# Kernel tuning notes

Measured on AMD Instinct MI355X. Metric: run time of the kernel, lower is better.

## Reference

```python
import jax, jax.numpy as jnp
import numpy as np

NUM_AGENTS = 16


def setup_inputs() -> dict:
    key = jax.random.key(0)
    ks = jax.random.split(key, 9)
    B, N, C = 64, 1024, 512
    w_scale = 1.0 / np.sqrt(C)  # keep pre-softmax logits in a sane range
    return {
        "x": jax.random.normal(ks[0], (B, N, C), dtype=jnp.float32),
        "Wq": jax.random.normal(ks[1], (C, C), dtype=jnp.float32) * w_scale,
        "bq": jax.random.normal(ks[2], (C,), dtype=jnp.float32) * 0.02,
        "Wk": jax.random.normal(ks[3], (C, C), dtype=jnp.float32) * w_scale,
        "bk": jax.random.normal(ks[4], (C,), dtype=jnp.float32) * 0.02,
        "Wv": jax.random.normal(ks[5], (C, C), dtype=jnp.float32) * w_scale,
        "bv": jax.random.normal(ks[6], (C,), dtype=jnp.float32) * 0.02,
        "Wo": jax.random.normal(ks[7], (C, C), dtype=jnp.float32) * w_scale,
        "bo": jax.random.normal(ks[8], (C,), dtype=jnp.float32) * 0.02,
    }


def reference(x, Wq, bq, Wk, bk, Wv, bv, Wo, bo):
    B, N, C = x.shape
    M = NUM_AGENTS
    scale = C ** (-0.5)
    # torch nn.Linear: y = x @ W.T + b
    Q = jnp.einsum('bnc,dc->bnd', x, Wq) + bq  # [B,N,C]
    K = jnp.einsum('bnc,dc->bnd', x, Wk) + bk
    V = jnp.einsum('bnc,dc->bnd', x, Wv) + bv
    # adaptive_avg_pool1d over token dim; N % M == 0 -> mean over groups of N//M
    A = Q.reshape(B, M, N // M, C).mean(axis=2)  # [B,M,C]
    # stage 1: softmax(Q A^T)
    agent_tokens = jax.nn.softmax(jnp.einsum('bnc,bmc->bnm', Q, A) * scale, axis=-1)  # [B,N,M]
    # stage 2: softmax(A K^T) V
    agent_features = jax.nn.softmax(jnp.einsum('bmc,bnc->bmn', A, K) * scale, axis=-1)  # [B,M,N]
    agent_features = jnp.einsum('bmn,bnc->bmc', agent_features, V)  # [B,M,C]
    # combine
    agent_attn = jnp.einsum('bnm,bmc->bnc', agent_tokens, agent_features)  # [B,N,C]
    return jnp.einsum('bnc,dc->bnd', agent_attn, Wo) + bo
```

## Files before the change

### kernel.cpp

```cpp
#include <hip/hip_runtime.h>

#define BB 64
#define NN 1024
#define CC 512
#define MM 16
#define SCALE 0.04419417382415922f

__device__ __forceinline__ float dot4(float4 a, float4 b) {
  return a.x*b.x + a.y*b.y + a.z*b.z + a.w*b.w;
}

__global__ void k_pool2(const float* __restrict__ x, float* __restrict__ P) {
  __shared__ float4 tmp[128];
  int blk = blockIdx.x;
  int t = threadIdx.x;
  int c4 = t & 127, h = t >> 7;
  const float4* base = (const float4*)(x + (size_t)blk * 64 * CC);
  float4 a = {0.f,0.f,0.f,0.f};
  #pragma unroll 8
  for (int i = 0; i < 32; ++i) {
    float4 v = base[(size_t)(h*32 + i)*128 + c4];
    a.x += v.x; a.y += v.y; a.z += v.z; a.w += v.w;
  }
  if (h == 1) tmp[c4] = a;
  __syncthreads();
  if (h == 0) {
    float4 o = tmp[c4];
    const float inv = 1.0f/64.0f;
    float4 r = {(a.x+o.x)*inv, (a.y+o.y)*inv, (a.z+o.z)*inv, (a.w+o.w)*inv};
    ((float4*)P)[(size_t)blk*128 + c4] = r;
  }
}

__global__ void k_gemm_nt(const float* __restrict__ In, const float* __restrict__ W,
                          const float* __restrict__ bias, float* __restrict__ Out) {
  int t = threadIdx.x;
  int tx = t & 15, ty = t >> 4;
  int r0 = blockIdx.y*32 + ty*2;
  int d0 = blockIdx.x*32 + tx*2;
  const float4* In4 = (const float4*)In;
  const float4* W4  = (const float4*)W;
  float acc00=0.f, acc01=0.f, acc10=0.f, acc11=0.f;
  for (int c4 = 0; c4 < 128; ++c4) {
    float4 a0 = In4[(size_t)r0*128 + c4];
    float4 a1 = In4[(size_t)(r0+1)*128 + c4];
    float4 w0 = W4[(size_t)d0*128 + c4];
    float4 w1 = W4[(size_t)(d0+1)*128 + c4];
    acc00 += dot4(a0,w0); acc01 += dot4(a0,w1);
    acc10 += dot4(a1,w0); acc11 += dot4(a1,w1);
  }
  float b0 = bias[d0], b1 = bias[d0+1];
  float2 o0 = {acc00+b0, acc01+b1};
  float2 o1 = {acc10+b0, acc11+b1};
  *(float2*)(Out + (size_t)r0*CC + d0) = o0;
  *(float2*)(Out + (size_t)(r0+1)*CC + d0) = o1;
}

__global__ void k_abqk(const float* __restrict__ A, const float* __restrict__ bq,
                       const float* __restrict__ bk, float* __restrict__ abq,
                       float* __restrict__ abk) {
  int bm = blockIdx.x, t = threadIdx.x;
  float sq = 0.f, sk = 0.f;
  for (int d = t; d < CC; d += 64) {
    float a = A[(size_t)bm*CC + d];
    sq += a*bq[d]; sk += a*bk[d];
  }
  #pragma unroll
  for (int off = 32; off >= 1; off >>= 1) {
    sq += __shfl_xor(sq, off);
    sk += __shfl_xor(sk, off);
  }
  if (t == 0) { abq[bm] = sq; abk[bm] = sk; }
}

__global__ void k_gemm_nn2(const float* __restrict__ A, const float* __restrict__ Wq,
                           const float* __restrict__ Wk, float* __restrict__ Aq,
                           float* __restrict__ Ak) {
  int t = threadIdx.x;
  int tx = t & 15, ty = t >> 4;
  int r0 = blockIdx.y*32 + ty*2;
  int c0 = blockIdx.x*32 + tx*2;
  float q00=0.f,q01=0.f,q10=0.f,q11=0.f;
  float k00=0.f,k01=0.f,k10=0.f,k11=0.f;
  #pragma unroll 4
  for (int d = 0; d < CC; ++d) {
    float a0 = A[(size_t)r0*CC + d];
    float a1 = A[(size_t)(r0+1)*CC + d];
    float2 wq = *(const float2*)(Wq + (size_t)d*CC + c0);
    float2 wk = *(const float2*)(Wk + (size_t)d*CC + c0);
    q00 += a0*wq.x; q01 += a0*wq.y; q10 += a1*wq.x; q11 += a1*wq.y;
    k00 += a0*wk.x; k01 += a0*wk.y; k10 += a1*wk.x; k11 += a1*wk.y;
  }
  float2 v;
  v.x=q00; v.y=q01; *(float2*)(Aq + (size_t)r0*CC + c0) = v;
  v.x=q10; v.y=q11; *(float2*)(Aq + (size_t)(r0+1)*CC + c0) = v;
  v.x=k00; v.y=k01; *(float2*)(Ak + (size_t)r0*CC + c0) = v;
  v.x=k10; v.y=k11; *(float2*)(Ak + (size_t)(r0+1)*CC + c0) = v;
}

__global__ __launch_bounds__(128) void k_logits3(
    const float* __restrict__ x, const float* __restrict__ Aq,
    const float* __restrict__ Ak, const float* __restrict__ abq,
    const float* __restrict__ abk, float* __restrict__ PT,
    float* __restrict__ E, float* __restrict__ dpart) {
  __shared__ float4 xs[128*17];
  __shared__ float ds[MM*132];
  __shared__ float ds2[MM*8];
  int b = blockIdx.y, t = threadIdx.x;
  int n0 = blockIdx.x*128;
  int n = n0 + t;
  const float4* Aq4 = (const float4*)(Aq + (size_t)b*MM*CC);
  const float4* Ak4 = (const float4*)(Ak + (size_t)b*MM*CC);
  const float4* xg  = (const float4*)(x + ((size_t)b*NN + n0)*CC);
  float aq[MM], ak[MM];
  #pragma unroll
  for (int m = 0; m < MM; ++m) { aq[m] = 0.f; ak[m] = 0.f; }
  for (int ch = 0; ch < 8; ++ch) {
    __syncthreads();
    #pragma unroll
    for (int j = 0; j < 16; ++j) {
      int i = j*128 + t;
      int row = i >> 4, col = i & 15;
      xs[row*17 + col] = xg[(size_t)row*128 + ch*16 + col];
    }
    __syncthreads();
    int cb = ch*16;
    #pragma unroll 4
    for (int c4 = 0; c4 < 16; ++c4) {
      float4 xv = xs[t*17 + c4];
      #pragma unroll
      for (int m = 0; m < MM; ++m) {
        aq[m] += dot4(xv, Aq4[m*128 + cb + c4]);
        ak[m] += dot4(xv, Ak4[m*128 + cb + c4]);
      }
    }
  }
  float mx = -1e30f;
  #pragma unroll
  for (int m = 0; m < MM; ++m) {
    aq[m] = SCALE*(aq[m] + abq[b*MM + m]);
    mx = fmaxf(mx, aq[m]);
  }
  float s = 0.f;
  #pragma unroll
  for (int m = 0; m < MM; ++m) { aq[m] = expf(aq[m]-mx); s += aq[m]; }
  float inv = 1.0f/s;
  float4* PT4 = (float4*)(PT + ((size_t)b*NN + n)*MM);
  #pragma unroll
  for (int j = 0; j < 4; ++j) {
    float4 v = {aq[j*4+0]*inv, aq[j*4+1]*inv, aq[j*4+2]*inv, aq[j*4+3]*inv};
    PT4[j] = v;
  }
  #pragma unroll
  for (int m = 0; m < MM; ++m) {
    float e = expf(SCALE*(ak[m] + abk[b*MM + m]));
    E[((size_t)b*MM + m)*NN + n] = e;
    ds[m*132 + t] = e;
  }
  __syncthreads();
  {
    int m2 = t >> 3, j2 = t & 7;
    float p = 0.f;
    #pragma unroll
    for (int i = 0; i < 16; ++i) p += ds[m2*132 + j2*16 + i];
    ds2[m2*8 + j2] = p;
  }
  __syncthreads();
  if (t < MM) {
    float d = 0.f;
    #pragma unroll
    for (int j = 0; j < 8; ++j) d += ds2[t*8 + j];
    dpart[((size_t)blockIdx.x*BB + b)*MM + t] = d;
  }
}

__global__ __launch_bounds__(256) void k_sacc3(const float* __restrict__ x,
                                               const float* __restrict__ E,
                                               float* __restrict__ Spart) {
  __shared__ float Es[MM*128];
  __shared__ float4 comb[MM*128];
  int ns = blockIdx.x, b = blockIdx.y, t = threadIdx.x;
  int col = t & 127, h = t >> 7;
  {
    const float4* E4 = (const float4*)E;
    float4* Es4 = (float4*)Es;
    #pragma unroll
    for (int k = 0; k < 2; ++k) {
      int i = k*256 + t;
      int m = i >> 5, j = i & 31;
      Es4[m*32 + j] = E4[((size_t)b*MM + m)*256 + ns*32 + j];
    }
  }
  __syncthreads();
  float4 acc[MM];
  #pragma unroll
  for (int m = 0; m < MM; ++m) acc[m] = make_float4(0.f,0.f,0.f,0.f);
  const float4* xb = (const float4*)(x + ((size_t)b*NN + ns*128 + h*64)*CC);
  for (int nl = 0; nl < 64; ++nl) {
    float4 xv = xb[(size_t)nl*128 + col];
    #pragma unroll
    for (int m = 0; m < MM; ++m) {
      float p = Es[m*128 + h*64 + nl];
      acc[m].x += p*xv.x; acc[m].y += p*xv.y; acc[m].z += p*xv.z; acc[m].w += p*xv.w;
    }
  }
  if (h == 1) {
    #pragma unroll
    for (int m = 0; m < MM; ++m) comb[m*128 + col] = acc[m];
  }
  __syncthreads();
  if (h == 0) {
    float4* Sp4 = (float4*)Spart;
    #pragma unroll
    for (int m = 0; m < MM; ++m) {
      float4 c = comb[m*128 + col];
      float4 r = {acc[m].x+c.x, acc[m].y+c.y, acc[m].z+c.z, acc[m].w+c.w};
      Sp4[(((size_t)ns*BB + b)*MM + m)*128 + col] = r;
    }
  }
}

__global__ void k_sreduce2(const float* __restrict__ Spart,
                           const float* __restrict__ dpart,
                           float* __restrict__ S) {
  int idx = blockIdx.x*256 + threadIdx.x;
  int row = idx >> 7;
  const float4* Sp4 = (const float4*)Spart;
  float4 a = {0.f,0.f,0.f,0.f};
  #pragma unroll
  for (int ns = 0; ns < 8; ++ns) {
    float4 v = Sp4[((size_t)ns*NN + row)*128 + (idx & 127)];
    a.x += v.x; a.y += v.y; a.z += v.z; a.w += v.w;
  }
  float d = 0.f;
  #pragma unroll
  for (int ns = 0; ns < 8; ++ns) d += dpart[(size_t)ns*NN + row];
  float inv = 1.0f/d;
  float4 r = {a.x*inv, a.y*inv, a.z*inv, a.w*inv};
  ((float4*)S)[idx] = r;
}

__global__ __launch_bounds__(128) void k_final3(const float* __restrict__ PT,
                                                const float* __restrict__ G,
                                                float* __restrict__ out) {
  int nc = blockIdx.x, b = blockIdx.y, t = threadIdx.x;
  float4 g[MM];
  const float4* G4 = (const float4*)(G + (size_t)b*MM*CC);
  #pragma unroll
  for (int m = 0; m < MM; ++m) g[m] = G4[m*128 + t];
  int n0 = nc*32;
  float4* out4 = (float4*)(out + ((size_t)b*NN + n0)*CC);
  const float* pt = PT + ((size_t)b*NN + n0)*MM;
  for (int i = 0; i < 32; ++i) {
    float4 o = {0.f,0.f,0.f,0.f};
    #pragma unroll
    for (int m = 0; m < MM; ++m) {
      float p = pt[i*MM + m];
      o.x += p*g[m].x; o.y += p*g[m].y; o.z += p*g[m].z; o.w += p*g[m].w;
    }
    out4[(size_t)i*128 + t] = o;
  }
}

extern "C" void kernel_launch(void* const* d_in, const int* in_sizes, int n_in,
                              void* d_out, int out_size, void* d_ws, size_t ws_size,
                              hipStream_t stream) {
  (void)in_sizes; (void)n_in; (void)out_size; (void)ws_size;
  const float* x  = (const float*)d_in[0];
  const float* Wq = (const float*)d_in[1];
  const float* bq = (const float*)d_in[2];
  const float* Wk = (const float*)d_in[3];
  const float* bk = (const float*)d_in[4];
  const float* Wv = (const float*)d_in[5];
  const float* bv = (const float*)d_in[6];
  const float* Wo = (const float*)d_in[7];
  const float* bo = (const float*)d_in[8];
  float* out = (float*)d_out;

  float* ws  = (float*)d_ws;
  float* P     = ws;
  float* A     = P  + 1024*512;
  float* Aq    = A  + 1024*512;
  float* Ak    = Aq + 1024*512;
  float* abq   = Ak + 1024*512;
  float* abk   = abq + 1024;
  float* PT    = abk + 1024;
  float* E     = PT + 1024*1024;
  float* dpart = E  + 1024*1024;
  float* S     = dpart + 8*1024;
  float* AF    = S  + 1024*512;
  float* G     = AF + 1024*512;
  float* Spart = G  + 1024*512;

  k_pool2<<<1024, 256, 0, stream>>>(x, P);
  k_gemm_nt<<<dim3(16,32), 256, 0, stream>>>(P, Wq, bq, A);
  k_abqk<<<1024, 64, 0, stream>>>(A, bq, bk, abq, abk);
  k_gemm_nn2<<<dim3(16,32), 256, 0, stream>>>(A, Wq, Wk, Aq, Ak);
  k_logits3<<<dim3(8,64), 128, 0, stream>>>(x, Aq, Ak, abq, abk, PT, E, dpart);
  k_sacc3<<<dim3(8,64), 256, 0, stream>>>(x, E, Spart);
  k_sreduce2<<<512, 256, 0, stream>>>(Spart, dpart, S);
  k_gemm_nt<<<dim3(16,32), 256, 0, stream>>>(S, Wv, bv, AF);
  k_gemm_nt<<<dim3(16,32), 256, 0, stream>>>(AF, Wo, bo, G);
  k_final3<<<dim3(32,64), 128, 0, stream>>>(PT, G, out);
}
```

Baseline: 760.5 us.

## Split logits over channel chunks, move softmax into sacc, retile small GEMMs

The logits kernel is split across four channel chunks (grid z) that write partial Q/K logits, which raises parallelism beyond 512 blocks. The softmax, exp and denominator work moves into the S-accumulation kernel, which sums the partials, so the E buffer round trip is gone. The small GEMMs are rewritten to stage input rows in shared memory with more blocks and coalesced weight reads. The final kernel uses smaller token chunks for more blocks. The cost is extra partial-logit traffic and redundant reloading of x per channel chunk.

Result: no change. 759.0 us (-0.2%).

```diff
diff --git a/kernel.cpp b/kernel.cpp
--- a/kernel.cpp
+++ b/kernel.cpp
@@ -8,6 +8,9 @@
 
 __device__ __forceinline__ float dot4(float4 a, float4 b) {
   return a.x*b.x + a.y*b.y + a.z*b.z + a.w*b.w;
+}
+__device__ __forceinline__ void fma4(float4& acc, float s, float4 v) {
+  acc.x += s*v.x; acc.y += s*v.y; acc.z += s*v.z; acc.w += s*v.w;
 }
 
 __global__ void k_pool2(const float* __restrict__ x, float* __restrict__ P) {
@@ -32,28 +35,35 @@
   }
 }
 
-__global__ void k_gemm_nt(const float* __restrict__ In, const float* __restrict__ W,
-                          const float* __restrict__ bias, float* __restrict__ Out) {
+__global__ __launch_bounds__(256) void k_gemm_nt3(const float* __restrict__ In,
+    const float* __restrict__ W, const float* __restrict__ bias,
+    float* __restrict__ Out) {
+  __shared__ float4 As[8*128];
   int t = threadIdx.x;
-  int tx = t & 15, ty = t >> 4;
-  int r0 = blockIdx.y*32 + ty*2;
-  int d0 = blockIdx.x*32 + tx*2;
+  int rblk = blockIdx.y, dblk = blockIdx.x;
   const float4* In4 = (const float4*)In;
-  const float4* W4  = (const float4*)W;
-  float acc00=0.f, acc01=0.f, acc10=0.f, acc11=0.f;
+  #pragma unroll
+  for (int k = 0; k < 4; ++k) {
+    int i = k*256 + t;
+    As[i] = In4[(size_t)(rblk*8 + (i>>7))*128 + (i&127)];
+  }
+  __syncthreads();
+  int d = dblk*64 + (t & 63);
+  int rr = t >> 6;
+  const float4* Wr = (const float4*)W + (size_t)d*128;
+  const float4* A0 = &As[(rr*2)*128];
+  const float4* A1 = &As[(rr*2+1)*128];
+  float acc0 = 0.f, acc1 = 0.f;
+  #pragma unroll 4
   for (int c4 = 0; c4 < 128; ++c4) {
-    float4 a0 = In4[(size_t)r0*128 + c4];
-    float4 a1 = In4[(size_t)(r0+1)*128 + c4];
-    float4 w0 = W4[(size_t)d0*128 + c4];
-    float4 w1 = W4[(size_t)(d0+1)*128 + c4];
-    acc00 += dot4(a0,w0); acc01 += dot4(a0,w1);
-    acc10 += dot4(a1,w0); acc11 += dot4(a1,w1);
-  }
-  float b0 = bias[d0], b1 = bias[d0+1];
-  float2 o0 = {acc00+b0, acc01+b1};
-  float2 o1 = {acc10+b0, acc11+b1};
-  *(float2*)(Out + (size_t)r0*CC + d0) = o0;
-  *(float2*)(Out + (size_t)(r0+1)*CC + d0) = o1;
+    float4 w = Wr[c4];
+    acc0 += dot4(A0[c4], w);
+    acc1 += dot4(A1[c4], w);
+  }
+  float bv = bias[d];
+  int r0 = rblk*8 + rr*2;
+  Out[(size_t)r0*CC + d] = acc0 + bv;
+  Out[(size_t)(r0+1)*CC + d] = acc1 + bv;
 }
 
 __global__ void k_abqk(const float* __restrict__ A, const float* __restrict__ bq,
@@ -73,58 +83,59 @@
   if (t == 0) { abq[bm] = sq; abk[bm] = sk; }
 }
 
-__global__ void k_gemm_nn2(const float* __restrict__ A, const float* __restrict__ Wq,
-                           const float* __restrict__ Wk, float* __restrict__ Aq,
-                           float* __restrict__ Ak) {
+__global__ __launch_bounds__(256) void k_gemm_nn3(const float* __restrict__ A,
+    const float* __restrict__ Wq, const float* __restrict__ Wk,
+    float* __restrict__ Aq, float* __restrict__ Ak) {
+  __shared__ float As[4*512];
   int t = threadIdx.x;
-  int tx = t & 15, ty = t >> 4;
-  int r0 = blockIdx.y*32 + ty*2;
-  int c0 = blockIdx.x*32 + tx*2;
-  float q00=0.f,q01=0.f,q10=0.f,q11=0.f;
-  float k00=0.f,k01=0.f,k10=0.f,k11=0.f;
-  #pragma unroll 4
-  for (int d = 0; d < CC; ++d) {
-    float a0 = A[(size_t)r0*CC + d];
-    float a1 = A[(size_t)(r0+1)*CC + d];
-    float2 wq = *(const float2*)(Wq + (size_t)d*CC + c0);
-    float2 wk = *(const float2*)(Wk + (size_t)d*CC + c0);
-    q00 += a0*wq.x; q01 += a0*wq.y; q10 += a1*wq.x; q11 += a1*wq.y;
-    k00 += a0*wk.x; k01 += a0*wk.y; k10 += a1*wk.x; k11 += a1*wk.y;
-  }
-  float2 v;
-  v.x=q00; v.y=q01; *(float2*)(Aq + (size_t)r0*CC + c0) = v;
-  v.x=q10; v.y=q11; *(float2*)(Aq + (size_t)(r0+1)*CC + c0) = v;
-  v.x=k00; v.y=k01; *(float2*)(Ak + (size_t)r0*CC + c0) = v;
-  v.x=k10; v.y=k11; *(float2*)(Ak + (size_t)(r0+1)*CC + c0) = v;
-}
-
-__global__ __launch_bounds__(128) void k_logits3(
-    const float* __restrict__ x, const float* __restrict__ Aq,
-    const float* __restrict__ Ak, const float* __restrict__ abq,
-    const float* __restrict__ abk, float* __restrict__ PT,
-    float* __restrict__ E, float* __restrict__ dpart) {
+  int rblk = blockIdx.y, cblk = blockIdx.x;
+  const float4* A4 = (const float4*)A;
+  float4* As4 = (float4*)As;
+  #pragma unroll
+  for (int k = 0; k < 2; ++k) {
+    int i = k*256 + t;
+    As4[i] = A4[(size_t)(rblk*4 + (i>>7))*128 + (i&127)];
+  }
+  __syncthreads();
+  int c4 = cblk*64 + (t & 63);
+  int rr = t >> 6;
+  const float* Ar = &As[rr*512];
+  const float4* Wq4 = (const float4*)Wq;
+  const float4* Wk4 = (const float4*)Wk;
+  float4 accq = {0.f,0.f,0.f,0.f}, acck = {0.f,0.f,0.f,0.f};
+  #pragma unroll 8
+  for (int d = 0; d < 512; ++d) {
+    float a = Ar[d];
+    fma4(accq, a, Wq4[(size_t)d*128 + c4]);
+    fma4(acck, a, Wk4[(size_t)d*128 + c4]);
+  }
+  int row = rblk*4 + rr;
+  ((float4*)Aq)[(size_t)row*128 + c4] = accq;
+  ((float4*)Ak)[(size_t)row*128 + c4] = acck;
+}
+
+__global__ __launch_bounds__(128) void k_logits4(const float* __restrict__ x,
+    const float* __restrict__ Aq, const float* __restrict__ Ak,
+    float* __restrict__ Pq, float* __restrict__ Pk) {
   __shared__ float4 xs[128*17];
-  __shared__ float ds[MM*132];
-  __shared__ float ds2[MM*8];
-  int b = blockIdx.y, t = threadIdx.x;
+  int b = blockIdx.y, t = threadIdx.x, cz = blockIdx.z;
   int n0 = blockIdx.x*128;
-  int n = n0 + t;
   const float4* Aq4 = (const float4*)(Aq + (size_t)b*MM*CC);
   const float4* Ak4 = (const float4*)(Ak + (size_t)b*MM*CC);
   const float4* xg  = (const float4*)(x + ((size_t)b*NN + n0)*CC);
   float aq[MM], ak[MM];
   #pragma unroll
   for (int m = 0; m < MM; ++m) { aq[m] = 0.f; ak[m] = 0.f; }
-  for (int ch = 0; ch < 8; ++ch) {
+  for (int ch = 0; ch < 2; ++ch) {
     __syncthreads();
     #pragma unroll
     for (int j = 0; j < 16; ++j) {
       int i = j*128 + t;
       int row = i >> 4, col = i & 15;
-      xs[row*17 + col] = xg[(size_t)row*128 + ch*16 + col];
+      xs[row*17 + col] = xg[(size_t)row*128 + cz*32 + ch*16 + col];
     }
     __syncthreads();
-    int cb = ch*16;
+    int cb = cz*32 + ch*16;
     #pragma unroll 4
     for (int c4 = 0; c4 < 16; ++c4) {
       float4 xv = xs[t*17 + c4];
@@ -135,74 +146,105 @@
       }
     }
   }
-  float mx = -1e30f;
-  #pragma unroll
-  for (int m = 0; m < MM; ++m) {
-    aq[m] = SCALE*(aq[m] + abq[b*MM + m]);
-    mx = fmaxf(mx, aq[m]);
-  }
-  float s = 0.f;
-  #pragma unroll
-  for (int m = 0; m < MM; ++m) { aq[m] = expf(aq[m]-mx); s += aq[m]; }
-  float inv = 1.0f/s;
-  float4* PT4 = (float4*)(PT + ((size_t)b*NN + n)*MM);
+  int n = n0 + t;
+  float4* Pq4 = (float4*)Pq + (((size_t)cz*BB + b)*NN + n)*4;
+  float4* Pk4 = (float4*)Pk + (((size_t)cz*BB + b)*NN + n)*4;
   #pragma unroll
   for (int j = 0; j < 4; ++j) {
-    float4 v = {aq[j*4+0]*inv, aq[j*4+1]*inv, aq[j*4+2]*inv, aq[j*4+3]*inv};
-    PT4[j] = v;
-  }
-  #pragma unroll
-  for (int m = 0; m < MM; ++m) {
-    float e = expf(SCALE*(ak[m] + abk[b*MM + m]));
-    E[((size_t)b*MM + m)*NN + n] = e;
-    ds[m*132 + t] = e;
-  }
-  __syncthreads();
-  {
-    int m2 = t >> 3, j2 = t & 7;
-    float p = 0.f;
-    #pragma unroll
-    for (int i = 0; i < 16; ++i) p += ds[m2*132 + j2*16 + i];
-    ds2[m2*8 + j2] = p;
-  }
-  __syncthreads();
-  if (t < MM) {
-    float d = 0.f;
-    #pragma unroll
-    for (int j = 0; j < 8; ++j) d += ds2[t*8 + j];
-    dpart[((size_t)blockIdx.x*BB + b)*MM + t] = d;
-  }
-}
-
-__global__ __launch_bounds__(256) void k_sacc3(const float* __restrict__ x,
-                                               const float* __restrict__ E,
-                                               float* __restrict__ Spart) {
+    float4 v = {aq[j*4+0], aq[j*4+1], aq[j*4+2], aq[j*4+3]};
+    Pq4[j] = v;
+    float4 w = {ak[j*4+0], ak[j*4+1], ak[j*4+2], ak[j*4+3]};
+    Pk4[j] = w;
+  }
+}
+
+__global__ __launch_bounds__(256) void k_sacc4(const float* __restrict__ x,
+    const float* __restrict__ Pq, const float* __restrict__ Pk,
+    const float* __restrict__ abq, const float* __restrict__ abk,
+    float* __restrict__ PT, float* __restrict__ dpart,
+    float* __restrict__ Spart) {
   __shared__ float Es[MM*128];
   __shared__ float4 comb[MM*128];
+  __shared__ float ds2[128];
   int ns = blockIdx.x, b = blockIdx.y, t = threadIdx.x;
+  int n0 = ns*128;
+  if (t < 128) {
+    int n = n0 + t;
+    float4 s[4];
+    #pragma unroll
+    for (int j = 0; j < 4; ++j) s[j] = make_float4(0.f,0.f,0.f,0.f);
+    #pragma unroll
+    for (int cz = 0; cz < 4; ++cz) {
+      const float4* Pk4 = (const float4*)Pk + (((size_t)cz*BB + b)*NN + n)*4;
+      #pragma unroll
+      for (int j = 0; j < 4; ++j) {
+        float4 v = Pk4[j];
+        s[j].x += v.x; s[j].y += v.y; s[j].z += v.z; s[j].w += v.w;
+      }
+    }
+    #pragma unroll
+    for (int j = 0; j < 4; ++j) {
+      Es[(j*4+0)*128 + t] = expf(SCALE*(s[j].x + abk[b*MM + j*4+0]));
+      Es[(j*4+1)*128 + t] = expf(SCALE*(s[j].y + abk[b*MM + j*4+1]));
+      Es[(j*4+2)*128 + t] = expf(SCALE*(s[j].z + abk[b*MM + j*4+2]));
+      Es[(j*4+3)*128 + t] = expf(SCALE*(s[j].w + abk[b*MM + j*4+3]));
+    }
+  } else {
+    int n = n0 + (t - 128);
+    float a[MM];
+    #pragma unroll
+    for (int m = 0; m < MM; ++m) a[m] = 0.f;
+    #pragma unroll
+    for (int cz = 0; cz < 4; ++cz) {
+      const float4* Pq4 = (const float4*)Pq + (((size_t)cz*BB + b)*NN + n)*4;
+      #pragma unroll
+      for (int j = 0; j < 4; ++j) {
+        float4 v = Pq4[j];
+        a[j*4+0] += v.x; a[j*4+1] += v.y; a[j*4+2] += v.z; a[j*4+3] += v.w;
+      }
+    }
+    float mx = -1e30f;
+    #pragma unroll
+    for (int m = 0; m < MM; ++m) {
+      a[m] = SCALE*(a[m] + abq[b*MM + m]);
+      mx = fmaxf(mx, a[m]);
+    }
+    float ssum = 0.f;
+    #pragma unroll
+    for (int m = 0; m < MM; ++m) { a[m] = expf(a[m]-mx); ssum += a[m]; }
+    float inv = 1.0f/ssum;
+    float4* PT4 = (float4*)PT + ((size_t)b*NN + n)*4;
+    #pragma unroll
+    for (int j = 0; j < 4; ++j) {
+      float4 v = {a[j*4+0]*inv, a[j*4+1]*inv, a[j*4+2]*inv, a[j*4+3]*inv};
+      PT4[j] = v;
+    }
+  }
+  __syncthreads();
+  if (t < 128) {
+    int m = t >> 3, j = t & 7;
+    float p = 0.f;
+    #pragma unroll
+    for (int i = 0; i < 16; ++i) p += Es[m*128 + j*16 + i];
+    ds2[t] = p;
+  }
+  __syncthreads();
+  if (t < MM) {
+    float dsum = 0.f;
+    #pragma unroll
+    for (int j = 0; j < 8; ++j) dsum += ds2[t*8 + j];
+    dpart[((size_t)ns*BB + b)*MM + t] = dsum;
+  }
   int col = t & 127, h = t >> 7;
-  {
-    const float4* E4 = (const float4*)E;
-    float4* Es4 = (float4*)Es;
-    #pragma unroll
-    for (int k = 0; k < 2; ++k) {
-      int i = k*256 + t;
-      int m = i >> 5, j = i & 31;
-      Es4[m*32 + j] = E4[((size_t)b*MM + m)*256 + ns*32 + j];
-    }
-  }
-  __syncthreads();
   float4 acc[MM];
   #pragma unroll
   for (int m = 0; m < MM; ++m) acc[m] = make_float4(0.f,0.f,0.f,0.f);
-  const float4* xb = (const float4*)(x + ((size_t)b*NN + ns*128 + h*64)*CC);
+  const float4* xb = (const float4*)(x + ((size_t)b*NN + n0 + h*64)*CC);
   for (int nl = 0; nl < 64; ++nl) {
     float4 xv = xb[(size_t)nl*128 + col];
     #pragma unroll
-    for (int m = 0; m < MM; ++m) {
-      float p = Es[m*128 + h*64 + nl];
-      acc[m].x += p*xv.x; acc[m].y += p*xv.y; acc[m].z += p*xv.z; acc[m].w += p*xv.w;
-    }
+    for (int m = 0; m < MM; ++m)
+      fma4(acc[m], Es[m*128 + h*64 + nl], xv);
   }
   if (h == 1) {
     #pragma unroll
@@ -240,7 +282,7 @@
   ((float4*)S)[idx] = r;
 }
 
-__global__ __launch_bounds__(128) void k_final3(const float* __restrict__ PT,
+__global__ __launch_bounds__(128) void k_final4(const float* __restrict__ PT,
                                                 const float* __restrict__ G,
                                                 float* __restrict__ out) {
   int nc = blockIdx.x, b = blockIdx.y, t = threadIdx.x;
@@ -248,10 +290,10 @@
   const float4* G4 = (const float4*)(G + (size_t)b*MM*CC);
   #pragma unroll
   for (int m = 0; m < MM; ++m) g[m] = G4[m*128 + t];
-  int n0 = nc*32;
+  int n0 = nc*16;
   float4* out4 = (float4*)(out + ((size_t)b*NN + n0)*CC);
   const float* pt = PT + ((size_t)b*NN + n0)*MM;
-  for (int i = 0; i < 32; ++i) {
+  for (int i = 0; i < 16; ++i) {
     float4 o = {0.f,0.f,0.f,0.f};
     #pragma unroll
     for (int m = 0; m < MM; ++m) {
@@ -285,21 +327,22 @@
   float* abq   = Ak + 1024*512;
   float* abk   = abq + 1024;
   float* PT    = abk + 1024;
-  float* E     = PT + 1024*1024;
-  float* dpart = E  + 1024*1024;
+  float* dpart = PT + 1024*1024;
   float* S     = dpart + 8*1024;
   float* AF    = S  + 1024*512;
   float* G     = AF + 1024*512;
   float* Spart = G  + 1024*512;
+  float* Pq    = Spart + 8*1024*512;
+  float* Pk    = Pq + 4*1024*1024/4*4;
 
   k_pool2<<<1024, 256, 0, stream>>>(x, P);
-  k_gemm_nt<<<dim3(16,32), 256, 0, stream>>>(P, Wq, bq, A);
+  k_gemm_nt3<<<dim3(8,128), 256, 0, stream>>>(P, Wq, bq, A);
   k_abqk<<<1024, 64, 0, stream>>>(A, bq, bk, abq, abk);
-  k_gemm_nn2<<<dim3(16,32), 256, 0, stream>>>(A, Wq, Wk, Aq, Ak);
-  k_logits3<<<dim3(8,64), 128, 0, stream>>>(x, Aq, Ak, abq, abk, PT, E, dpart);
-  k_sacc3<<<dim3(8,64), 256, 0, stream>>>(x, E, Spart);
+  k_gemm_nn3<<<dim3(2,256), 256, 0, stream>>>(A, Wq, Wk, Aq, Ak);
+  k_logits4<<<dim3(8,64,4), 128, 0, stream>>>(x, Aq, Ak, Pq, Pk);
+  k_sacc4<<<dim3(8,64), 256, 0, stream>>>(x, Pq, Pk, abq, abk, PT, dpart, Spart);
   k_sreduce2<<<512, 256, 0, stream>>>(Spart, dpart, S);
-  k_gemm_nt<<<dim3(16,32), 256, 0, stream>>>(S, Wv, bv, AF);
-  k_gemm_nt<<<dim3(16,32), 256, 0, stream>>>(AF, Wo, bo, G);
-  k_final3<<<dim3(32,64), 128, 0, stream>>>(PT, G, out);
-}
+  k_gemm_nt3<<<dim3(8,128), 256, 0, stream>>>(S, Wv, bv, AF);
+  k_gemm_nt3<<<dim3(8,128), 256, 0, stream>>>(AF, Wo, bo, G);
+  k_final4<<<dim3(64,64), 128, 0, stream>>>(PT, G, out);
+}
```
